# Optimization experiments

Hardware: AMD Instinct MI355X
Metric: run time of the kernel (lower is better)

## Reference

```python
import jax, jax.numpy as jnp
import numpy as np

DOWN = 4
FOCAL_A, FOCAL_B = 2.0, 4.0
RAD_ALPHA = 0.54
HM_W, WH_W = 1.0, 0.1
B, NUM_CLASSES, H, W = 16, 80, 128, 128
MAX_OBJ, N_VALID = 100, 60


def setup_inputs() -> dict:
    key = jax.random.key(0)
    k1, k2, k3, k4, k5, k6, k7, k8 = jax.random.split(key, 8)
    heatmap_heads = jax.random.normal(k1, (B, NUM_CLASSES, H, W), dtype=jnp.float32)
    # wh heads are non-negative distances (l,t,r,b) in input-image pixels
    wh_heads = jax.random.uniform(k2, (B, 4, H, W), dtype=jnp.float32) * 32.0
    # synthetic COCO-style annotations: (x1,y1,x2,y2,cls), cls=-1 pads
    x1 = jax.random.uniform(k3, (B, MAX_OBJ)) * 400.0
    y1 = jax.random.uniform(k4, (B, MAX_OBJ)) * 400.0
    bw = 16.0 + jax.random.uniform(k5, (B, MAX_OBJ)) * 96.0
    bh = 16.0 + jax.random.uniform(k6, (B, MAX_OBJ)) * 96.0
    x2 = jnp.minimum(x1 + bw, 511.0)
    y2 = jnp.minimum(y1 + bh, 511.0)
    cls = jax.random.randint(k7, (B, MAX_OBJ), 0, NUM_CLASSES).astype(jnp.float32)
    cls = jnp.where(jnp.arange(MAX_OBJ)[None, :] < N_VALID, cls, -1.0)
    annotations = jnp.stack([x1, y1, x2, y2, cls], axis=-1).astype(jnp.float32)
    return {"heatmap_heads": heatmap_heads, "wh_heads": wh_heads, "annotations": annotations}


def _single_targets(annots, num_classes, height, width):
    # annots: [N,5]; replicates TTFNet per-image target generation, vectorized.
    boxes = annots[:, :4]
    cls = annots[:, 4]
    valid = cls >= 0
    areas = (boxes[:, 3] - boxes[:, 1] + 1.0) * (boxes[:, 2] - boxes[:, 0] + 1.0)
    log_a = jnp.where(valid, jnp.log(jnp.maximum(areas, 1e-12)), -jnp.inf)
    order = jnp.argsort(-log_a)
    boxes, cls, valid = boxes[order], cls[order], valid[order]
    cx = jnp.trunc((boxes[:, 0] + boxes[:, 2]) * 0.5 / DOWN)
    cy = jnp.trunc((boxes[:, 1] + boxes[:, 3]) * 0.5 / DOWN)
    fx1 = jnp.clip(boxes[:, 0] / DOWN, 0.0, width - 1)
    fx2 = jnp.clip(boxes[:, 2] / DOWN, 0.0, width - 1)
    fy1 = jnp.clip(boxes[:, 1] / DOWN, 0.0, height - 1)
    fy2 = jnp.clip(boxes[:, 3] / DOWN, 0.0, height - 1)
    hr = ((fy2 - fy1) * 0.5 * RAD_ALPHA).astype(jnp.int32)  # .int() trunc (coords >= 0)
    wr = ((fx2 - fx1) * 0.5 * RAD_ALPHA).astype(jnp.int32)
    sx = (2 * wr + 1).astype(jnp.float32) / 6.0  # sigma_x = w/6
    sy = (2 * hr + 1).astype(jnp.float32) / 6.0  # sigma_y = h/6
    xs = jnp.arange(width, dtype=jnp.float32)
    ys = jnp.arange(height, dtype=jnp.float32)
    dx = xs[None, :] - cx[:, None]  # [N,W]
    dy = ys[None, :] - cy[:, None]  # [N,H]
    gx = jnp.where((jnp.abs(dx) <= wr[:, None]) & valid[:, None],
                   jnp.exp(-(dx * dx) / (2.0 * sx[:, None] * sx[:, None])), 0.0)
    gy = jnp.where(jnp.abs(dy) <= hr[:, None],
                   jnp.exp(-(dy * dy) / (2.0 * sy[:, None] * sy[:, None])), 0.0)
    g = gy[:, :, None] * gx[:, None, :]  # [N,H,W] truncated gaussian per box
    cls_idx = jnp.clip(cls.astype(jnp.int32), 0, num_classes - 1)
    hm = jnp.zeros((num_classes, height, width), jnp.float32).at[cls_idx].max(g)
    n = g.shape[0]
    idx = jnp.arange(n)[:, None, None]
    owner = jnp.max(jnp.where(g > 0, idx, -1), axis=0)  # last (smallest) box covering each pixel
    covered = owner >= 0
    oc = jnp.clip(owner, 0)
    box_t = jnp.where(covered[None], jnp.transpose(boxes[oc], (2, 0, 1)), -1.0)  # [4,H,W]
    gsum = jnp.maximum(g.sum(axis=(1, 2)), 1e-12)
    wnorm = g / gsum[:, None, None]  # local_heatmap / ct_div (boxes_area_topk_log is forced to 1.0)
    reg = jnp.where(covered, jnp.take_along_axis(wnorm, oc[None], axis=0)[0], 0.0)[None]  # [1,H,W]
    return hm, box_t, reg


def _forward(heatmap_heads, wh_heads, annotations):
    b, num_classes, height, width = heatmap_heads.shape
    hm_t, box_t, reg_w = jax.vmap(lambda a: _single_targets(a, num_classes, height, width))(annotations)
    hm_t = jax.lax.stop_gradient(hm_t)
    box_t = jax.lax.stop_gradient(box_t)
    reg_w = jax.lax.stop_gradient(reg_w)

    pred = jax.nn.sigmoid(heatmap_heads).transpose(0, 2, 3, 1).reshape(b, -1, num_classes)
    wh = wh_heads.transpose(0, 2, 3, 1).reshape(b, -1, 4)
    tgt = hm_t.transpose(0, 2, 3, 1).reshape(b, -1, num_classes)
    boxes = box_t.transpose(0, 2, 3, 1).reshape(b, -1, 4)
    w = reg_w.transpose(0, 2, 3, 1).reshape(b, -1)

    # focal (CornerNet-style) heatmap loss
    pos = (tgt == 1.0).astype(jnp.float32)
    neg = (tgt < 1.0).astype(jnp.float32)
    neg_wt = (1.0 - tgt) ** FOCAL_B
    pos_loss = jnp.sum(-jnp.log(pred) * (1.0 - pred) ** FOCAL_A * pos)
    neg_loss = jnp.sum(-jnp.log(1.0 - pred) * pred ** FOCAL_A * neg_wt * neg)
    num_pos = pos.sum()
    hm_loss = jnp.where(num_pos > 0, (pos_loss + neg_loss) / num_pos, neg_loss) * HM_W

    # decode predicted boxes on feature grid (stride = down_ratio)
    shift_y, shift_x = jnp.meshgrid(jnp.arange(height, dtype=jnp.float32) * DOWN,
                                    jnp.arange(width, dtype=jnp.float32) * DOWN, indexing='ij')
    base = jnp.stack([shift_x, shift_y], axis=-1).reshape(-1, 2)  # [HW,2]
    pred_boxes = jnp.concatenate([base[None] - wh[:, :, :2], base[None] + wh[:, :, 2:]], axis=2)

    avg_factor = w.sum() + 1e-4
    m = w > 0
    safe = jnp.array([0.0, 0.0, 1.0, 1.0], jnp.float32)
    p = jnp.where(m[..., None], pred_boxes, safe)
    t = jnp.where(m[..., None], boxes, safe)
    lt = jnp.maximum(p[..., :2], t[..., :2])
    rb = jnp.minimum(p[..., 2:], t[..., 2:])
    wh_i = jnp.clip(rb - lt + 1.0, 0.0)
    e1 = jnp.minimum(p[..., :2], t[..., :2])
    e2 = jnp.maximum(p[..., 2:], t[..., 2:])
    ewh = jnp.clip(e2 - e1 + 1.0, 0.0)
    overlap = wh_i[..., 0] * wh_i[..., 1]
    ap = (p[..., 2] - p[..., 0] + 1.0) * (p[..., 3] - p[..., 1] + 1.0)
    ag = (t[..., 2] - t[..., 0] + 1.0) * (t[..., 3] - t[..., 1] + 1.0)
    u = ap + ag - overlap
    ious = overlap / u
    e_area = ewh[..., 0] * ewh[..., 1]
    gious = ious - (e_area - u) / e_area
    wh_loss = (jnp.sum((1.0 - gious) * w) / avg_factor)[None] * WH_W
    return hm_loss, wh_loss


def reference(heatmap_heads, wh_heads, annotations):
    return _forward(heatmap_heads, wh_heads, annotations)
```

## Files before the change

### kernel.cpp

```cpp
#include <hip/hip_runtime.h>
#include <math.h>

#define NB 16
#define NC 80
#define HH 128
#define WW 128
#define NOBJ 100
#define HW (HH*WW)
#define SCATTER_BLOCKS (NB*NOBJ)
#define F4_TOTAL (NB*NC*HW/4)
#define F4_PER_BLOCK (256*8)
#define DENSE_BLOCKS (F4_TOTAL/F4_PER_BLOCK)
#define TOTAL_BLOCKS (SCATTER_BLOCKS + DENSE_BLOCKS)
#define DENSE_SLOTS 64

#define NV_OFF 1152
#define PAR_OFF 1216

__global__ __launch_bounds__(128) void prep_kernel(const float* __restrict__ ann,
                                                   double* __restrict__ acc,
                                                   int* __restrict__ nv,
                                                   float4* __restrict__ par) {
    int b = blockIdx.x;
    int i = threadIdx.x;
    __shared__ float skey[128];
    __shared__ int s_nv;
    if (i == 0) s_nv = 0;

    if (i < 5) acc[i * 16 + b] = 0.0;
    if (i >= 8 && i < 12) acc[80 + b * 4 + (i - 8)] = 0.0;

    float x1=0.f, y1=0.f, x2=0.f, y2=0.f, clsv=-1.f;
    float key = INFINITY;
    if (i < NOBJ) {
        const float* a = ann + ((size_t)b * NOBJ + i) * 5;
        x1=a[0]; y1=a[1]; x2=a[2]; y2=a[3]; clsv=a[4];
        if (clsv >= 0.f) {
            float area = (y2 - y1 + 1.f) * (x2 - x1 + 1.f);
            key = -__logf(fmaxf(area, 1e-12f));
        }
    }
    skey[i] = key;
    __syncthreads();

    if (i < NOBJ) {
        int r = 0;
        for (int j = 0; j < NOBJ; ++j) {
            float kj = skey[j];
            if (kj < key || (kj == key && j < i)) r++;
        }
        bool valid = (clsv >= 0.f);
        if (valid) atomicAdd(&s_nv, 1);

        float cx = truncf((x1 + x2) * 0.125f);
        float cy = truncf((y1 + y2) * 0.125f);
        float fx1 = fminf(fmaxf(x1*0.25f, 0.f), WW - 1.f);
        float fx2 = fminf(fmaxf(x2*0.25f, 0.f), WW - 1.f);
        float fy1 = fminf(fmaxf(y1*0.25f, 0.f), HH - 1.f);
        float fy2 = fminf(fmaxf(y2*0.25f, 0.f), HH - 1.f);
        int hr = (int)((fy2 - fy1) * 0.5f * 0.54f);
        int wr = (int)((fx2 - fx1) * 0.5f * 0.54f);
        float sx = (float)(2*wr + 1) / 6.0f;
        float sy = (float)(2*hr + 1) / 6.0f;
        float ivx = 1.f / (2.f * sx * sx);
        float ivy = 1.f / (2.f * sy * sy);

        int yc = (int)cy, xc = (int)cx;
        float sgy = 0.f;
        {
            int ya = max(0, yc - hr), yb = min(HH - 1, yc + hr);
            for (int y = ya; y <= yb; ++y) {
                float dy = (float)y - cy;
                sgy += __expf(-(dy*dy) * ivy);
            }
        }
        float sgx = 0.f;
        if (valid) {
            int xa = max(0, xc - wr), xb = min(WW - 1, xc + wr);
            for (int x = xa; x <= xb; ++x) {
                float dx = (float)x - cx;
                sgx += __expf(-(dx*dx) * ivx);
            }
        }
        float gsum = fmaxf(sgy * sgx, 1e-12f);
        int cls_i = min(max((int)clsv, 0), NC - 1);

        size_t o = ((size_t)b * NOBJ + (size_t)r) * 3;
        par[o + 0] = make_float4(cx, cy, (float)wr, (float)hr);
        par[o + 1] = make_float4(ivx, ivy, __int_as_float(cls_i), 1.f / gsum);
        par[o + 2] = make_float4(x1, y1, x2, y2);
    }
    __syncthreads();
    if (i == 0) nv[b] = s_nv;
}

__global__ __launch_bounds__(256) void main_kernel(const float* __restrict__ heat,
                                                   const float* __restrict__ wh,
                                                   const float4* __restrict__ par,
                                                   const int* __restrict__ nv,
                                                   double* __restrict__ acc) {
    if (blockIdx.x >= SCATTER_BLOCKS) {
        int db = blockIdx.x - SCATTER_BLOCKS;
        const float4* hp = (const float4*)heat;
        size_t base = (size_t)db * F4_PER_BLOCK + threadIdx.x;
        float4 v[8];
        #pragma unroll
        for (int k = 0; k < 8; ++k) v[k] = hp[base + (size_t)k * 256];
        float n0 = 0.f, n1 = 0.f;
        #pragma unroll
        for (int k = 0; k < 8; ++k) {
            float hv[4] = { v[k].x, v[k].y, v[k].z, v[k].w };
            #pragma unroll
            for (int m = 0; m < 4; ++m) {
                float h = hv[m];
                float e = __expf(-h);
                float q = 1.f + e;
                float lq = __logf(q);
                float p = 1.f / q;
                float t = (h + lq) * p * p;
                if (m & 1) n1 += t; else n0 += t;
            }
        }
        float r = n0 + n1;
        for (int off = 32; off > 0; off >>= 1) r += __shfl_down(r, off, 64);
        __shared__ float dred[4];
        int lane = threadIdx.x & 63, wv = threadIdx.x >> 6;
        if (lane == 0) dred[wv] = r;
        __syncthreads();
        if (threadIdx.x == 0) {
            double s = (double)dred[0] + (double)dred[1] + (double)dred[2] + (double)dred[3];
            atomicAdd(&acc[80 + (db & (DENSE_SLOTS - 1))], s);
        }
        return;
    }

    int s = blockIdx.x;
    int b = s / NOBJ;
    int i = s - b * NOBJ;
    int nvb = nv[b];
    if (i >= nvb) return;

    __shared__ float4 sobj[NOBJ][3];
    {
        const float4* src = par + (size_t)b * NOBJ * 3;
        float4* dst = &sobj[0][0];
        for (int t = threadIdx.x; t < NOBJ * 3; t += 256) dst[t] = src[t];
    }
    __syncthreads();

    float4 g0i = sobj[i][0], g1i = sobj[i][1], g2i = sobj[i][2];
    float cx = g0i.x, cy = g0i.y;
    int wr = (int)g0i.z, hr = (int)g0i.w;
    float ivx = g1i.x, ivy = g1i.y;
    int ci = __float_as_int(g1i.z);
    float ivg = g1i.w;
    int xc = (int)cx, yc = (int)cy;
    int xa = max(0, xc - wr), xb = min(WW - 1, xc + wr);
    int ya = max(0, yc - hr), yb = min(HH - 1, yc + hr);
    int wN = xb - xa + 1, hN = yb - ya + 1, npix = wN * hN;

    float posl = 0.f, negl = 0.f, npos = 0.f, wsum = 0.f, gl = 0.f;

    for (int t0 = threadIdx.x; t0 < npix; t0 += 256) {
        int ry = t0 / wN;
        int px = xa + (t0 - ry * wN);
        int py = ya + ry;
        float fx = (float)px, fy = (float)py;

        bool first = true;
        for (int j = 0; j < i; ++j) {
            float4 g1 = sobj[j][1];
            if (__float_as_int(g1.z) != ci) continue;
            float4 g0 = sobj[j][0];
            if (fabsf(fx - g0.x) <= g0.z && fabsf(fy - g0.y) <= g0.w) { first = false; break; }
        }

        float dxi = fx - cx, dyi = fy - cy;
        float gi = __expf(-(dxi*dxi) * ivx) * __expf(-(dyi*dyi) * ivy);
        float t = gi;
        bool is_owner = true;
        for (int j = i + 1; j < nvb; ++j) {
            float4 g0 = sobj[j][0];
            float dxj = fx - g0.x, dyj = fy - g0.y;
            if (fabsf(dxj) <= g0.z && fabsf(dyj) <= g0.w) {
                is_owner = false;
                if (first) {
                    float4 g1 = sobj[j][1];
                    if (__float_as_int(g1.z) == ci) {
                        float gj = __expf(-(dxj*dxj) * g1.x) * __expf(-(dyj*dyj) * g1.y);
                        t = fmaxf(t, gj);
                    }
                }
            }
        }

        if (first) {
            float h = heat[((size_t)b * NC + ci) * HW + (size_t)py * WW + px];
            float e = __expf(-h);
            float q = 1.f + e;
            float lq = __logf(q);
            float p = 1.f / q;
            float basef = (h + lq) * p * p;
            if (t == 1.0f) {
                posl += lq * (1.f - p) * (1.f - p);
                negl -= basef;
                npos += 1.f;
            } else {
                float u1 = 1.f - t;
                float u2 = u1 * u1;
                negl += basef * (u2 * u2 - 1.f);
            }
        }

        if (is_owner) {
            float w = gi * ivg;
            size_t po = (size_t)py * WW + px;
            const float* whb = wh + (size_t)b * 4 * HW + po;
            float w0 = whb[0], w1 = whb[HW], w2 = whb[2*HW], w3 = whb[3*HW];
            float bx = fx * 4.f, by = fy * 4.f;
            float px1 = bx - w0, py1 = by - w1, px2 = bx + w2, py2 = by + w3;
            float tx1 = g2i.x, ty1 = g2i.y, tx2 = g2i.z, ty2 = g2i.w;
            float ltx = fmaxf(px1, tx1), lty = fmaxf(py1, ty1);
            float rbx = fminf(px2, tx2), rby = fminf(py2, ty2);
            float iw = fmaxf(rbx - ltx + 1.f, 0.f), ih = fmaxf(rby - lty + 1.f, 0.f);
            float e1x = fminf(px1, tx1), e1y = fminf(py1, ty1);
            float e2x = fmaxf(px2, tx2), e2y = fmaxf(py2, ty2);
            float ew = fmaxf(e2x - e1x + 1.f, 0.f), eh = fmaxf(e2y - e1y + 1.f, 0.f);
            float ov = iw * ih;
            float ap = (px2 - px1 + 1.f) * (py2 - py1 + 1.f);
            float ag = (tx2 - tx1 + 1.f) * (ty2 - ty1 + 1.f);
            float u = ap + ag - ov;
            float iou = ov / u;
            float ea = ew * eh;
            float giou = iou - (ea - u) / ea;
            wsum += w;
            gl += (1.f - giou) * w;
        }
    }

    float vals[5] = { posl, negl, npos, wsum, gl };
    #pragma unroll
    for (int k = 0; k < 5; ++k) {
        float v = vals[k];
        for (int off = 32; off > 0; off >>= 1) v += __shfl_down(v, off, 64);
        vals[k] = v;
    }
    __shared__ float red[5][4];
    int lane = threadIdx.x & 63, wv = threadIdx.x >> 6;
    if (lane == 0) {
        #pragma unroll
        for (int k = 0; k < 5; ++k) red[k][wv] = vals[k];
    }
    __syncthreads();
    if (threadIdx.x == 0) {
        #pragma unroll
        for (int k = 0; k < 5; ++k) {
            double vsum = (double)red[k][0] + (double)red[k][1] + (double)red[k][2] + (double)red[k][3];
            atomicAdd(&acc[k * 16 + b], vsum);
        }
    }
}

__global__ void finalize_kernel(const double* __restrict__ acc, float* __restrict__ out) {
    double posl=0, negc=0, npos=0, wsum=0, gl=0, dneg=0;
    for (int b = 0; b < NB; ++b) {
        posl += acc[0*16 + b];
        negc += acc[1*16 + b];
        npos += acc[2*16 + b];
        wsum += acc[3*16 + b];
        gl   += acc[4*16 + b];
    }
    for (int k = 0; k < DENSE_SLOTS; ++k) dneg += acc[80 + k];
    double neg = negc + dneg;
    double hm = (npos > 0.0) ? (posl + neg) / npos : neg;
    out[0] = (float)hm;
    out[1] = (float)(gl / (wsum + 1e-4) * 0.1);
}

extern "C" void kernel_launch(void* const* d_in, const int* in_sizes, int n_in,
                              void* d_out, int out_size, void* d_ws, size_t ws_size,
                              hipStream_t stream) {
    const float* heat = (const float*)d_in[0];
    const float* wh   = (const float*)d_in[1];
    const float* ann  = (const float*)d_in[2];
    float* out = (float*)d_out;

    double* acc = (double*)d_ws;
    int*    nv  = (int*)((char*)d_ws + NV_OFF);
    float4* par = (float4*)((char*)d_ws + PAR_OFF);

    prep_kernel<<<NB, 128, 0, stream>>>(ann, acc, nv, par);
    main_kernel<<<TOTAL_BLOCKS, 256, 0, stream>>>(heat, wh, par, nv, acc);
    finalize_kernel<<<1, 1, 0, stream>>>(acc, out);
}
```

Before: 141.2 us.

## Fuse target prep into scatter blocks, prune overlap lists, drop atomics

Removes the separate prep kernel: each scatter block recomputes its image's sorted object parameters in shared memory. Each block then builds per-object lists of intersecting earlier same-class and later objects, so the per-pixel loops only visit candidates. Global double atomics are replaced by per-block partial slots, and finalize becomes a 256-thread parallel reduction. This trades one launch and the atomic contention for redundant per-block sorting work, up to 100x duplicated per image.

```diff
diff --git a/kernel.cpp b/kernel.cpp
--- a/kernel.cpp
+++ b/kernel.cpp
@@ -12,42 +12,79 @@
 #define F4_PER_BLOCK (256*8)
 #define DENSE_BLOCKS (F4_TOTAL/F4_PER_BLOCK)
 #define TOTAL_BLOCKS (SCATTER_BLOCKS + DENSE_BLOCKS)
-#define DENSE_SLOTS 64
-
-#define NV_OFF 1152
-#define PAR_OFF 1216
-
-__global__ __launch_bounds__(128) void prep_kernel(const float* __restrict__ ann,
-                                                   double* __restrict__ acc,
-                                                   int* __restrict__ nv,
-                                                   float4* __restrict__ par) {
-    int b = blockIdx.x;
-    int i = threadIdx.x;
-    __shared__ float skey[128];
-    __shared__ int s_nv;
-    if (i == 0) s_nv = 0;
-
-    if (i < 5) acc[i * 16 + b] = 0.0;
-    if (i >= 8 && i < 12) acc[80 + b * 4 + (i - 8)] = 0.0;
+
+#define SACC_OFF DENSE_BLOCKS
+
+__global__ __launch_bounds__(256, 4) void main_kernel(const float* __restrict__ heat,
+                                                      const float* __restrict__ wh,
+                                                      const float* __restrict__ ann,
+                                                      double* __restrict__ part) {
+    if (blockIdx.x >= SCATTER_BLOCKS) {
+        int db = blockIdx.x - SCATTER_BLOCKS;
+        const float4* hp = (const float4*)heat;
+        size_t base = (size_t)db * F4_PER_BLOCK + threadIdx.x;
+        float4 v[8];
+        #pragma unroll
+        for (int k = 0; k < 8; ++k) v[k] = hp[base + (size_t)k * 256];
+        float n0 = 0.f, n1 = 0.f;
+        #pragma unroll
+        for (int k = 0; k < 8; ++k) {
+            float hv[4] = { v[k].x, v[k].y, v[k].z, v[k].w };
+            #pragma unroll
+            for (int m = 0; m < 4; ++m) {
+                float h = hv[m];
+                float e = __expf(-h);
+                float q = 1.f + e;
+                float lq = __logf(q);
+                float p = 1.f / q;
+                float t = (h + lq) * p * p;
+                if (m & 1) n1 += t; else n0 += t;
+            }
+        }
+        float r = n0 + n1;
+        for (int off = 32; off > 0; off >>= 1) r += __shfl_down(r, off, 64);
+        __shared__ float dred[4];
+        int lane = threadIdx.x & 63, wv = threadIdx.x >> 6;
+        if (lane == 0) dred[wv] = r;
+        __syncthreads();
+        if (threadIdx.x == 0)
+            part[db] = (double)dred[0] + (double)dred[1] + (double)dred[2] + (double)dred[3];
+        return;
+    }
+
+    int sblk = blockIdx.x;
+    int b = sblk / NOBJ;
+    int i = sblk - b * NOBJ;
+    double* sacc = part + SACC_OFF + (size_t)sblk * 5;
+    int tid = threadIdx.x;
+
+    __shared__ float4 sg0[NOBJ];
+    __shared__ float4 sg1[NOBJ];
+    __shared__ float4 sg2[NOBJ];
+    __shared__ float skey[NOBJ];
+    __shared__ int prevl[NOBJ], nextl[NOBJ];
+    __shared__ int s_nv, s_np, s_nn;
+    if (tid == 0) { s_nv = 0; s_np = 0; s_nn = 0; }
 
     float x1=0.f, y1=0.f, x2=0.f, y2=0.f, clsv=-1.f;
     float key = INFINITY;
-    if (i < NOBJ) {
-        const float* a = ann + ((size_t)b * NOBJ + i) * 5;
+    bool on = tid < NOBJ;
+    if (on) {
+        const float* a = ann + ((size_t)b * NOBJ + tid) * 5;
         x1=a[0]; y1=a[1]; x2=a[2]; y2=a[3]; clsv=a[4];
         if (clsv >= 0.f) {
             float area = (y2 - y1 + 1.f) * (x2 - x1 + 1.f);
             key = -__logf(fmaxf(area, 1e-12f));
         }
-    }
-    skey[i] = key;
-    __syncthreads();
-
-    if (i < NOBJ) {
+        skey[tid] = key;
+    }
+    __syncthreads();
+
+    if (on) {
         int r = 0;
         for (int j = 0; j < NOBJ; ++j) {
             float kj = skey[j];
-            if (kj < key || (kj == key && j < i)) r++;
+            if (kj < key || (kj == key && j < tid)) r++;
         }
         bool valid = (clsv >= 0.f);
         if (valid) atomicAdd(&s_nv, 1);
@@ -85,70 +122,19 @@
         float gsum = fmaxf(sgy * sgx, 1e-12f);
         int cls_i = min(max((int)clsv, 0), NC - 1);
 
-        size_t o = ((size_t)b * NOBJ + (size_t)r) * 3;
-        par[o + 0] = make_float4(cx, cy, (float)wr, (float)hr);
-        par[o + 1] = make_float4(ivx, ivy, __int_as_float(cls_i), 1.f / gsum);
-        par[o + 2] = make_float4(x1, y1, x2, y2);
-    }
-    __syncthreads();
-    if (i == 0) nv[b] = s_nv;
-}
-
-__global__ __launch_bounds__(256) void main_kernel(const float* __restrict__ heat,
-                                                   const float* __restrict__ wh,
-                                                   const float4* __restrict__ par,
-                                                   const int* __restrict__ nv,
-                                                   double* __restrict__ acc) {
-    if (blockIdx.x >= SCATTER_BLOCKS) {
-        int db = blockIdx.x - SCATTER_BLOCKS;
-        const float4* hp = (const float4*)heat;
-        size_t base = (size_t)db * F4_PER_BLOCK + threadIdx.x;
-        float4 v[8];
-        #pragma unroll
-        for (int k = 0; k < 8; ++k) v[k] = hp[base + (size_t)k * 256];
-        float n0 = 0.f, n1 = 0.f;
-        #pragma unroll
-        for (int k = 0; k < 8; ++k) {
-            float hv[4] = { v[k].x, v[k].y, v[k].z, v[k].w };
-            #pragma unroll
-            for (int m = 0; m < 4; ++m) {
-                float h = hv[m];
-                float e = __expf(-h);
-                float q = 1.f + e;
-                float lq = __logf(q);
-                float p = 1.f / q;
-                float t = (h + lq) * p * p;
-                if (m & 1) n1 += t; else n0 += t;
-            }
-        }
-        float r = n0 + n1;
-        for (int off = 32; off > 0; off >>= 1) r += __shfl_down(r, off, 64);
-        __shared__ float dred[4];
-        int lane = threadIdx.x & 63, wv = threadIdx.x >> 6;
-        if (lane == 0) dred[wv] = r;
-        __syncthreads();
-        if (threadIdx.x == 0) {
-            double s = (double)dred[0] + (double)dred[1] + (double)dred[2] + (double)dred[3];
-            atomicAdd(&acc[80 + (db & (DENSE_SLOTS - 1))], s);
-        }
+        sg0[r] = make_float4(cx, cy, (float)wr, (float)hr);
+        sg1[r] = make_float4(ivx, ivy, __int_as_float(cls_i), 1.f / gsum);
+        sg2[r] = make_float4(x1, y1, x2, y2);
+    }
+    __syncthreads();
+
+    int nvb = s_nv;
+    if (i >= nvb) {
+        if (tid < 5) sacc[tid] = 0.0;
         return;
     }
 
-    int s = blockIdx.x;
-    int b = s / NOBJ;
-    int i = s - b * NOBJ;
-    int nvb = nv[b];
-    if (i >= nvb) return;
-
-    __shared__ float4 sobj[NOBJ][3];
-    {
-        const float4* src = par + (size_t)b * NOBJ * 3;
-        float4* dst = &sobj[0][0];
-        for (int t = threadIdx.x; t < NOBJ * 3; t += 256) dst[t] = src[t];
-    }
-    __syncthreads();
-
-    float4 g0i = sobj[i][0], g1i = sobj[i][1], g2i = sobj[i][2];
+    float4 g0i = sg0[i], g1i = sg1[i], g2i = sg2[i];
     float cx = g0i.x, cy = g0i.y;
     int wr = (int)g0i.z, hr = (int)g0i.w;
     float ivx = g1i.x, ivy = g1i.y;
@@ -159,37 +145,51 @@
     int ya = max(0, yc - hr), yb = min(HH - 1, yc + hr);
     int wN = xb - xa + 1, hN = yb - ya + 1, npix = wN * hN;
 
+    if (tid < nvb && tid != i) {
+        float4 g0 = sg0[tid];
+        bool inter = (g0.x - g0.z <= (float)xb) && (g0.x + g0.z >= (float)xa) &&
+                     (g0.y - g0.w <= (float)yb) && (g0.y + g0.w >= (float)ya);
+        if (inter) {
+            int cj = __float_as_int(sg1[tid].z);
+            if (tid < i) {
+                if (cj == ci) prevl[atomicAdd(&s_np, 1)] = tid;
+            } else {
+                nextl[atomicAdd(&s_nn, 1)] = tid | ((cj == ci) ? 0x10000 : 0);
+            }
+        }
+    }
+    __syncthreads();
+    int np = s_np, nn = s_nn;
+
     float posl = 0.f, negl = 0.f, npos = 0.f, wsum = 0.f, gl = 0.f;
 
-    for (int t0 = threadIdx.x; t0 < npix; t0 += 256) {
+    for (int t0 = tid; t0 < npix; t0 += 256) {
         int ry = t0 / wN;
         int px = xa + (t0 - ry * wN);
         int py = ya + ry;
         float fx = (float)px, fy = (float)py;
 
         bool first = true;
-        for (int j = 0; j < i; ++j) {
-            float4 g1 = sobj[j][1];
-            if (__float_as_int(g1.z) != ci) continue;
-            float4 g0 = sobj[j][0];
-            if (fabsf(fx - g0.x) <= g0.z && fabsf(fy - g0.y) <= g0.w) { first = false; break; }
+        for (int k = 0; k < np; ++k) {
+            float4 g0 = sg0[prevl[k]];
+            if (fabsf(fx - g0.x) <= g0.z && fabsf(fy - g0.y) <= g0.w) first = false;
         }
 
         float dxi = fx - cx, dyi = fy - cy;
         float gi = __expf(-(dxi*dxi) * ivx) * __expf(-(dyi*dyi) * ivy);
         float t = gi;
         bool is_owner = true;
-        for (int j = i + 1; j < nvb; ++j) {
-            float4 g0 = sobj[j][0];
+        for (int k = 0; k < nn; ++k) {
+            int e = nextl[k];
+            int j = e & 0xFFFF;
+            float4 g0 = sg0[j];
             float dxj = fx - g0.x, dyj = fy - g0.y;
             if (fabsf(dxj) <= g0.z && fabsf(dyj) <= g0.w) {
                 is_owner = false;
-                if (first) {
-                    float4 g1 = sobj[j][1];
-                    if (__float_as_int(g1.z) == ci) {
-                        float gj = __expf(-(dxj*dxj) * g1.x) * __expf(-(dyj*dyj) * g1.y);
-                        t = fmaxf(t, gj);
-                    }
+                if ((e & 0x10000) && first) {
+                    float4 g1 = sg1[j];
+                    float gj = __expf(-(dxj*dxj) * g1.x) * __expf(-(dyj*dyj) * g1.y);
+                    t = fmaxf(t, gj);
                 }
             }
         }
@@ -246,35 +246,53 @@
         vals[k] = v;
     }
     __shared__ float red[5][4];
-    int lane = threadIdx.x & 63, wv = threadIdx.x >> 6;
+    int lane = tid & 63, wv = tid >> 6;
     if (lane == 0) {
         #pragma unroll
         for (int k = 0; k < 5; ++k) red[k][wv] = vals[k];
     }
     __syncthreads();
-    if (threadIdx.x == 0) {
-        #pragma unroll
-        for (int k = 0; k < 5; ++k) {
-            double vsum = (double)red[k][0] + (double)red[k][1] + (double)red[k][2] + (double)red[k][3];
-            atomicAdd(&acc[k * 16 + b], vsum);
-        }
+    if (tid == 0) {
+        #pragma unroll
+        for (int k = 0; k < 5; ++k)
+            sacc[k] = (double)red[k][0] + (double)red[k][1] + (double)red[k][2] + (double)red[k][3];
     }
 }
 
-__global__ void finalize_kernel(const double* __restrict__ acc, float* __restrict__ out) {
-    double posl=0, negc=0, npos=0, wsum=0, gl=0, dneg=0;
-    for (int b = 0; b < NB; ++b) {
-        posl += acc[0*16 + b];
-        negc += acc[1*16 + b];
-        npos += acc[2*16 + b];
-        wsum += acc[3*16 + b];
-        gl   += acc[4*16 + b];
-    }
-    for (int k = 0; k < DENSE_SLOTS; ++k) dneg += acc[80 + k];
-    double neg = negc + dneg;
-    double hm = (npos > 0.0) ? (posl + neg) / npos : neg;
-    out[0] = (float)hm;
-    out[1] = (float)(gl / (wsum + 1e-4) * 0.1);
+__global__ __launch_bounds__(256) void finalize_kernel(const double* __restrict__ part,
+                                                       float* __restrict__ out) {
+    int tid = threadIdx.x;
+    double v[6] = {0,0,0,0,0,0};
+    for (int d = tid; d < DENSE_BLOCKS; d += 256) v[0] += part[d];
+    for (int s = tid; s < SCATTER_BLOCKS; s += 256) {
+        const double* p = part + SACC_OFF + (size_t)s * 5;
+        v[1] += p[0]; v[2] += p[1]; v[3] += p[2]; v[4] += p[3]; v[5] += p[4];
+    }
+    #pragma unroll
+    for (int k = 0; k < 6; ++k) {
+        double x = v[k];
+        for (int off = 32; off > 0; off >>= 1) x += __shfl_down(x, off, 64);
+        v[k] = x;
+    }
+    __shared__ double red[6][4];
+    int lane = tid & 63, wv = tid >> 6;
+    if (lane == 0) {
+        #pragma unroll
+        for (int k = 0; k < 6; ++k) red[k][wv] = v[k];
+    }
+    __syncthreads();
+    if (tid == 0) {
+        double dneg = red[0][0] + red[0][1] + red[0][2] + red[0][3];
+        double posl = red[1][0] + red[1][1] + red[1][2] + red[1][3];
+        double negc = red[2][0] + red[2][1] + red[2][2] + red[2][3];
+        double npos = red[3][0] + red[3][1] + red[3][2] + red[3][3];
+        double wsum = red[4][0] + red[4][1] + red[4][2] + red[4][3];
+        double gl   = red[5][0] + red[5][1] + red[5][2] + red[5][3];
+        double neg = negc + dneg;
+        double hm = (npos > 0.0) ? (posl + neg) / npos : neg;
+        out[0] = (float)hm;
+        out[1] = (float)(gl / (wsum + 1e-4) * 0.1);
+    }
 }
 
 extern "C" void kernel_launch(void* const* d_in, const int* in_sizes, int n_in,
@@ -285,11 +303,8 @@
     const float* ann  = (const float*)d_in[2];
     float* out = (float*)d_out;
 
-    double* acc = (double*)d_ws;
-    int*    nv  = (int*)((char*)d_ws + NV_OFF);
-    float4* par = (float4*)((char*)d_ws + PAR_OFF);
-
-    prep_kernel<<<NB, 128, 0, stream>>>(ann, acc, nv, par);
-    main_kernel<<<TOTAL_BLOCKS, 256, 0, stream>>>(heat, wh, par, nv, acc);
-    finalize_kernel<<<1, 1, 0, stream>>>(acc, out);
+    double* part = (double*)d_ws;
+
+    main_kernel<<<TOTAL_BLOCKS, 256, 0, stream>>>(heat, wh, ann, part);
+    finalize_kernel<<<1, 256, 0, stream>>>(part, out);
 }
```

After: 136.4 us. -3.3%, faster.
